# Performance work log

Measured on AMD Instinct MI355X. Metric: run time of the kernel, lower is better.

Reference implementation:

```python
import jax, jax.numpy as jnp
import numpy as np

C_IN, C_OUT, K, H = 64, 128, 27, 100000

def setup_inputs() -> dict:
    key = jax.random.key(0)
    k1, k2, k3 = jax.random.split(key, 3)
    data_in = jax.random.normal(k1, (1, C_IN, H, 1), dtype=jnp.float32)
    # neighbor index table: 27 neighbors per node; -1 would mean 'missing' (zero-padded)
    neigh = jax.random.randint(k2, (H, K), 0, H, dtype=jnp.int64)
    # conv weight, fan-in scaled init, stored [C_out, C_in, K]
    weight = jax.random.normal(k3, (C_OUT, C_IN, K), dtype=jnp.float32) / np.sqrt(C_IN * K)
    return {"data_in": data_in, "neigh": neigh, "weight": weight}

def reference(data_in, neigh, weight):
    # data_in: [1, C_in, H, 1] (ocnn layout) -> [C_in, H]
    x = data_in[0, :, :, 0]
    # octree2col: gather 27 neighbors per node -> [C_in, H, K]
    cols = x[:, neigh]
    # zero out missing neighbors (index < 0)
    cols = jnp.where(neigh[None, :, :] >= 0, cols, jnp.zeros((), dtype=cols.dtype))
    # GEMM over (C_in, K) fused with ReLU -> [C_out, H]
    out = jnp.einsum('chk,ock->oh', cols, weight)
    out = jax.nn.relu(out)
    return out[None, :, :, None]  # back to ocnn layout [1, C_out, H, 1]
```

## Files before the change

kernel.cpp:

```cpp
#include <hip/hip_runtime.h>
#include <hip/hip_bf16.h>

#define C_IN  64
#define C_OUT 128
#define KK    27
#define HH    100000
#define TB    1563
#define WB    108
#define NBLK  391

typedef __attribute__((ext_vector_type(8))) short s8v;
typedef __attribute__((ext_vector_type(4))) float f32x4;

__device__ inline unsigned short f2bf(float f) {
    __hip_bfloat16 h = __float2bfloat16(f);
    return *reinterpret_cast<unsigned short*>(&h);
}

__device__ inline void dma16(const void* g, void* l) {
    __builtin_amdgcn_global_load_lds((const __attribute__((address_space(1))) void*)g,
                                     (__attribute__((address_space(3))) void*)l, 16, 0, 0);
}

__global__ __launch_bounds__(256) void prep_kernel(const float* __restrict__ x,
                                                   const float* __restrict__ w,
                                                   unsigned short* __restrict__ xt,
                                                   unsigned short* __restrict__ wk) {
    const int tid = threadIdx.x;
    if (blockIdx.x < TB) {
        __shared__ __align__(16) unsigned short ts[64 * 72];
        const int hbase = blockIdx.x * 64;
        #pragma unroll
        for (int it = 0; it < 16; ++it) {
            int i = it * 256 + tid;
            int c = i >> 6, hl = i & 63;
            int hg = hbase + hl;
            float v = (hg < HH) ? x[(size_t)c * HH + hg] : 0.f;
            ts[hl * 72 + c] = f2bf(v);
        }
        __syncthreads();
        #pragma unroll
        for (int it = 0; it < 2; ++it) {
            int u = it * 256 + tid;
            int hl = u >> 3, part = u & 7;
            int hg = hbase + hl;
            if (hg < HH)
                *(int4*)&xt[(size_t)hg * 64 + part * 8] = *(const int4*)&ts[hl * 72 + part * 8];
        }
    } else {
        int b = blockIdx.x - TB;
        int base = b * 2048 + tid;
        #pragma unroll
        for (int j = 0; j < 8; ++j) {
            int t = base + j * 256;
            int jj = t & 63, o = (t >> 6) & 127, kx = t >> 13;
            int lc = (jj >> 3) ^ (o & 7);
            int c  = lc * 8 + (jj & 7);
            wk[t] = f2bf(w[(size_t)o * (C_IN * KK) + c * KK + kx]);
        }
    }
}

__global__ __launch_bounds__(256, 2) void conv_main(const unsigned short* __restrict__ xt,
                                                    const unsigned short* __restrict__ wk,
                                                    const int* __restrict__ neigh,
                                                    float* __restrict__ out) {
    __shared__ int neigh_s[256 * KK];
    __shared__ __align__(16) unsigned short w_s[2][128 * 64];

    const int tid  = threadIdx.x;
    const int wave = tid >> 6;
    const int lane = tid & 63;
    const int col  = lane & 15;
    const int quad = lane >> 4;
    const int hbase = blockIdx.x * 256;

    #pragma unroll
    for (int j = 0; j < KK; ++j) {
        int i = j * 256 + tid;
        int hl = i / KK, kx = i - hl * KK;
        int hg = hbase + hl;
        neigh_s[i] = (hg < HH) ? neigh[(size_t)hg * KK + kx] : -1;
    }

    {
        const unsigned short* src = wk;
        #pragma unroll
        for (int i = 0; i < 4; ++i) {
            int row_base = wave * 8 + i * 32;
            dma16(src + row_base * 64 + lane * 8, &w_s[0][row_base * 64]);
        }
    }

    f32x4 acc[8][4];
    #pragma unroll
    for (int mt = 0; mt < 8; ++mt)
        #pragma unroll
        for (int nt = 0; nt < 4; ++nt)
            acc[mt][nt] = (f32x4){0.f, 0.f, 0.f, 0.f};

    __syncthreads();

    int4 cur[2][4], nxt[2][4];
    const int pc_b = (quad * 8);
    auto loadB = [&](int kk, int4 (&frag)[2][4]) {
        #pragma unroll
        for (int nt = 0; nt < 4; ++nt) {
            int n = wave * 64 + nt * 16 + col;
            int idx = neigh_s[n * KK + kk];
            if (idx >= 0) {
                const unsigned short* base = xt + (size_t)idx * 64 + pc_b;
                frag[0][nt] = *(const int4*)(base);
                frag[1][nt] = *(const int4*)(base + 32);
            } else {
                frag[0][nt] = make_int4(0, 0, 0, 0);
                frag[1][nt] = make_int4(0, 0, 0, 0);
            }
        }
    };

    loadB(0, cur);

    int p = 0;
    #pragma unroll 1
    for (int k = 0; k < KK; ++k) {
        if (k + 1 < KK) {
            const unsigned short* src = wk + (size_t)(k + 1) * (C_OUT * C_IN);
            #pragma unroll
            for (int i = 0; i < 4; ++i) {
                int row_base = wave * 8 + i * 32;
                dma16(src + row_base * 64 + lane * 8, &w_s[p ^ 1][row_base * 64]);
            }
            loadB(k + 1, nxt);
        }

        #pragma unroll
        for (int ch = 0; ch < 2; ++ch) {
            const int pc = (ch * 4 + quad) ^ (col & 7);
            #pragma unroll
            for (int mt = 0; mt < 8; ++mt) {
                s8v a = *(const s8v*)&w_s[p][(mt * 16 + col) * 64 + pc * 8];
                #pragma unroll
                for (int nt = 0; nt < 4; ++nt) {
                    s8v b = __builtin_bit_cast(s8v, cur[ch][nt]);
                    acc[mt][nt] = __builtin_amdgcn_mfma_f32_16x16x32_bf16(a, b, acc[mt][nt], 0, 0, 0);
                }
            }
        }

        __syncthreads();
        #pragma unroll
        for (int ch = 0; ch < 2; ++ch)
            #pragma unroll
            for (int nt = 0; nt < 4; ++nt)
                cur[ch][nt] = nxt[ch][nt];
        p ^= 1;
    }

    #pragma unroll
    for (int mt = 0; mt < 8; ++mt) {
        #pragma unroll
        for (int nt = 0; nt < 4; ++nt) {
            int hg = hbase + wave * 64 + nt * 16 + col;
            if (hg < HH) {
                #pragma unroll
                for (int r = 0; r < 4; ++r) {
                    int o = mt * 16 + quad * 4 + r;
                    float v = acc[mt][nt][r];
                    out[(size_t)o * HH + hg] = v > 0.f ? v : 0.f;
                }
            }
        }
    }
}

extern "C" void kernel_launch(void* const* d_in, const int* in_sizes, int n_in,
                              void* d_out, int out_size, void* d_ws, size_t ws_size,
                              hipStream_t stream) {
    const float* data_in = (const float*)d_in[0];
    const int*   neigh   = (const int*)d_in[1];
    const float* weight  = (const float*)d_in[2];
    float* out = (float*)d_out;

    unsigned short* xt = (unsigned short*)d_ws;
    unsigned short* wk = xt + (size_t)HH * 64;

    prep_kernel<<<TB + WB, 256, 0, stream>>>(data_in, weight, xt, wk);
    conv_main<<<NBLK, 256, 0, stream>>>(xt, wk, neigh, out);
}
```

Measured before the change: 167.6 us.

## Halve per-block node tile to 128 and unroll k-loop by two for occupancy

Each block now covers 128 nodes instead of 256, which doubles the grid and halves the accumulator and B-fragment registers per wave. Launch bounds go from 2 to 3 blocks per CU. The k loop is manually unrolled by two with explicit ping-pong register buffers, so the per-iteration copy of next fragments into current ones is removed. The aim is more waves in flight to hide gather latency, at the cost of loading the weight tiles twice as many times in total and doing half the MFMA reuse of each A fragment.

```diff
diff --git a/kernel.cpp b/kernel.cpp
--- a/kernel.cpp
+++ b/kernel.cpp
@@ -7,7 +7,7 @@
 #define HH    100000
 #define TB    1563
 #define WB    108
-#define NBLK  391
+#define NBLK  782
 
 typedef __attribute__((ext_vector_type(8))) short s8v;
 typedef __attribute__((ext_vector_type(4))) float f32x4;
@@ -61,11 +61,11 @@
     }
 }
 
-__global__ __launch_bounds__(256, 2) void conv_main(const unsigned short* __restrict__ xt,
+__global__ __launch_bounds__(256, 3) void conv_main(const unsigned short* __restrict__ xt,
                                                     const unsigned short* __restrict__ wk,
                                                     const int* __restrict__ neigh,
                                                     float* __restrict__ out) {
-    __shared__ int neigh_s[256 * KK];
+    __shared__ int neigh_s[128 * KK];
     __shared__ __align__(16) unsigned short w_s[2][128 * 64];
 
     const int tid  = threadIdx.x;
@@ -73,95 +73,89 @@
     const int lane = tid & 63;
     const int col  = lane & 15;
     const int quad = lane >> 4;
-    const int hbase = blockIdx.x * 256;
+    const int hbase = blockIdx.x * 128;
 
-    #pragma unroll
-    for (int j = 0; j < KK; ++j) {
-        int i = j * 256 + tid;
+    for (int i = tid; i < 128 * KK; i += 256) {
         int hl = i / KK, kx = i - hl * KK;
         int hg = hbase + hl;
         neigh_s[i] = (hg < HH) ? neigh[(size_t)hg * KK + kx] : -1;
     }
 
-    {
-        const unsigned short* src = wk;
+    auto dmaW = [&](int k, int b) {
+        const unsigned short* src = wk + (size_t)k * (C_OUT * C_IN);
         #pragma unroll
         for (int i = 0; i < 4; ++i) {
             int row_base = wave * 8 + i * 32;
-            dma16(src + row_base * 64 + lane * 8, &w_s[0][row_base * 64]);
+            dma16(src + row_base * 64 + lane * 8, &w_s[b][row_base * 64]);
         }
+    };
+
+    dmaW(0, 0);
+
+    f32x4 acc[8][2];
+    #pragma unroll
+    for (int mt = 0; mt < 8; ++mt) {
+        acc[mt][0] = (f32x4){0.f, 0.f, 0.f, 0.f};
+        acc[mt][1] = (f32x4){0.f, 0.f, 0.f, 0.f};
     }
-
-    f32x4 acc[8][4];
-    #pragma unroll
-    for (int mt = 0; mt < 8; ++mt)
-        #pragma unroll
-        for (int nt = 0; nt < 4; ++nt)
-            acc[mt][nt] = (f32x4){0.f, 0.f, 0.f, 0.f};
 
     __syncthreads();
 
-    int4 cur[2][4], nxt[2][4];
-    const int pc_b = (quad * 8);
-    auto loadB = [&](int kk, int4 (&frag)[2][4]) {
+    const int pc_b = quad * 8;
+    auto loadB = [&](int kk, int4 (&B)[4]) {
         #pragma unroll
-        for (int nt = 0; nt < 4; ++nt) {
-            int n = wave * 64 + nt * 16 + col;
+        for (int nt = 0; nt < 2; ++nt) {
+            int n = wave * 32 + nt * 16 + col;
             int idx = neigh_s[n * KK + kk];
             if (idx >= 0) {
                 const unsigned short* base = xt + (size_t)idx * 64 + pc_b;
-                frag[0][nt] = *(const int4*)(base);
-                frag[1][nt] = *(const int4*)(base + 32);
+                B[nt]     = *(const int4*)(base);
+                B[2 + nt] = *(const int4*)(base + 32);
             } else {
-                frag[0][nt] = make_int4(0, 0, 0, 0);
-                frag[1][nt] = make_int4(0, 0, 0, 0);
+                B[nt]     = make_int4(0, 0, 0, 0);
+                B[2 + nt] = make_int4(0, 0, 0, 0);
             }
         }
     };
 
-    loadB(0, cur);
-
-    int p = 0;
-    #pragma unroll 1
-    for (int k = 0; k < KK; ++k) {
-        if (k + 1 < KK) {
-            const unsigned short* src = wk + (size_t)(k + 1) * (C_OUT * C_IN);
-            #pragma unroll
-            for (int i = 0; i < 4; ++i) {
-                int row_base = wave * 8 + i * 32;
-                dma16(src + row_base * 64 + lane * 8, &w_s[p ^ 1][row_base * 64]);
-            }
-            loadB(k + 1, nxt);
-        }
-
+    auto mfma_phase = [&](const unsigned short* wbuf, int4 (&B)[4]) {
         #pragma unroll
         for (int ch = 0; ch < 2; ++ch) {
             const int pc = (ch * 4 + quad) ^ (col & 7);
             #pragma unroll
             for (int mt = 0; mt < 8; ++mt) {
-                s8v a = *(const s8v*)&w_s[p][(mt * 16 + col) * 64 + pc * 8];
-                #pragma unroll
-                for (int nt = 0; nt < 4; ++nt) {
-                    s8v b = __builtin_bit_cast(s8v, cur[ch][nt]);
-                    acc[mt][nt] = __builtin_amdgcn_mfma_f32_16x16x32_bf16(a, b, acc[mt][nt], 0, 0, 0);
-                }
+                s8v a = *(const s8v*)&wbuf[(mt * 16 + col) * 64 + pc * 8];
+                acc[mt][0] = __builtin_amdgcn_mfma_f32_16x16x32_bf16(a, __builtin_bit_cast(s8v, B[ch * 2 + 0]), acc[mt][0], 0, 0, 0);
+                acc[mt][1] = __builtin_amdgcn_mfma_f32_16x16x32_bf16(a, __builtin_bit_cast(s8v, B[ch * 2 + 1]), acc[mt][1], 0, 0, 0);
             }
         }
+    };
 
+    int4 B0[4], B1[4];
+    loadB(0, B0);
+
+    #pragma unroll 1
+    for (int kb = 0; kb < 13; ++kb) {
+        int k = kb * 2;
+        dmaW(k + 1, 1);
+        loadB(k + 1, B1);
+        mfma_phase(w_s[0], B0);
         __syncthreads();
-        #pragma unroll
-        for (int ch = 0; ch < 2; ++ch)
-            #pragma unroll
-            for (int nt = 0; nt < 4; ++nt)
-                cur[ch][nt] = nxt[ch][nt];
-        p ^= 1;
+
+        if (k + 2 < KK) {
+            dmaW(k + 2, 0);
+            loadB(k + 2, B0);
+        }
+        mfma_phase(w_s[1], B1);
+        __syncthreads();
     }
+    mfma_phase(w_s[0], B0);
 
     #pragma unroll
     for (int mt = 0; mt < 8; ++mt) {
         #pragma unroll
-        for (int nt = 0; nt < 4; ++nt) {
-            int hg = hbase + wave * 64 + nt * 16 + col;
+        for (int nt = 0; nt < 2; ++nt) {
+            int hg = hbase + wave * 32 + nt * 16 + col;
             if (hg < HH) {
                 #pragma unroll
                 for (int r = 0; r < 4; ++r) {
```

Result: slower. 186.8 us (+11.5%).

## Replace LDS DMA weight loads with register-staged double buffer and manual barriers

Applied to the files above, without the earlier changes.

Weights are no longer loaded with global_load_lds DMA. They are loaded into registers, written to the alternate LDS buffer after each MFMA phase, and B gathers are prefetched two stages ahead. The loop is unrolled by two with ping-pong register sets, and __syncthreads is replaced by an lgkmcnt-only waitcnt plus s_barrier, so outstanding global loads are not drained at each barrier. This costs extra registers (weight staging and a second B set) and risks spills or lower occupancy under launch_bounds(256,2), plus redundant loads at the tail where the stage index is clamped.

```diff
diff --git a/kernel.cpp b/kernel.cpp
--- a/kernel.cpp
+++ b/kernel.cpp
@@ -12,14 +12,16 @@
 typedef __attribute__((ext_vector_type(8))) short s8v;
 typedef __attribute__((ext_vector_type(4))) float f32x4;
 
+#define LGKM0_BARRIER() do { \
+    __asm__ __volatile__("" ::: "memory"); \
+    __builtin_amdgcn_s_waitcnt(0xC07F); \
+    __builtin_amdgcn_s_barrier(); \
+    __asm__ __volatile__("" ::: "memory"); \
+} while (0)
+
 __device__ inline unsigned short f2bf(float f) {
     __hip_bfloat16 h = __float2bfloat16(f);
     return *reinterpret_cast<unsigned short*>(&h);
-}
-
-__device__ inline void dma16(const void* g, void* l) {
-    __builtin_amdgcn_global_load_lds((const __attribute__((address_space(1))) void*)g,
-                                     (__attribute__((address_space(3))) void*)l, 16, 0, 0);
 }
 
 __global__ __launch_bounds__(256) void prep_kernel(const float* __restrict__ x,
@@ -83,15 +85,6 @@
         neigh_s[i] = (hg < HH) ? neigh[(size_t)hg * KK + kx] : -1;
     }
 
-    {
-        const unsigned short* src = wk;
-        #pragma unroll
-        for (int i = 0; i < 4; ++i) {
-            int row_base = wave * 8 + i * 32;
-            dma16(src + row_base * 64 + lane * 8, &w_s[0][row_base * 64]);
-        }
-    }
-
     f32x4 acc[8][4];
     #pragma unroll
     for (int mt = 0; mt < 8; ++mt)
@@ -101,61 +94,81 @@
 
     __syncthreads();
 
-    int4 cur[2][4], nxt[2][4];
-    const int pc_b = (quad * 8);
-    auto loadB = [&](int kk, int4 (&frag)[2][4]) {
+    const unsigned short* xq = xt + quad * 8;
+
+    auto loadW = [&](int k, int4 (&W)[4]) {
+        const int4* src = (const int4*)(wk + (size_t)k * (C_OUT * C_IN));
+        #pragma unroll
+        for (int j = 0; j < 4; ++j) W[j] = src[j * 256 + tid];
+    };
+    auto writeW = [&](int p, int4 (&W)[4]) {
+        #pragma unroll
+        for (int j = 0; j < 4; ++j)
+            *(int4*)&w_s[p][(j * 256 + tid) * 8] = W[j];
+    };
+
+    auto loadB = [&](int kk, int4 (&B)[2][4]) {
         #pragma unroll
         for (int nt = 0; nt < 4; ++nt) {
             int n = wave * 64 + nt * 16 + col;
             int idx = neigh_s[n * KK + kk];
             if (idx >= 0) {
-                const unsigned short* base = xt + (size_t)idx * 64 + pc_b;
-                frag[0][nt] = *(const int4*)(base);
-                frag[1][nt] = *(const int4*)(base + 32);
+                const unsigned short* base = xq + (size_t)idx * 64;
+                B[0][nt] = *(const int4*)(base);
+                B[1][nt] = *(const int4*)(base + 32);
             } else {
-                frag[0][nt] = make_int4(0, 0, 0, 0);
-                frag[1][nt] = make_int4(0, 0, 0, 0);
+                B[0][nt] = make_int4(0, 0, 0, 0);
+                B[1][nt] = make_int4(0, 0, 0, 0);
             }
         }
     };
 
-    loadB(0, cur);
-
-    int p = 0;
-    #pragma unroll 1
-    for (int k = 0; k < KK; ++k) {
-        if (k + 1 < KK) {
-            const unsigned short* src = wk + (size_t)(k + 1) * (C_OUT * C_IN);
-            #pragma unroll
-            for (int i = 0; i < 4; ++i) {
-                int row_base = wave * 8 + i * 32;
-                dma16(src + row_base * 64 + lane * 8, &w_s[p ^ 1][row_base * 64]);
-            }
-            loadB(k + 1, nxt);
-        }
-
+    auto mfma_phase = [&](const unsigned short* wbuf, int4 (&B)[2][4]) {
         #pragma unroll
         for (int ch = 0; ch < 2; ++ch) {
             const int pc = (ch * 4 + quad) ^ (col & 7);
             #pragma unroll
             for (int mt = 0; mt < 8; ++mt) {
-                s8v a = *(const s8v*)&w_s[p][(mt * 16 + col) * 64 + pc * 8];
+                s8v a = *(const s8v*)&wbuf[(mt * 16 + col) * 64 + pc * 8];
                 #pragma unroll
-                for (int nt = 0; nt < 4; ++nt) {
-                    s8v b = __builtin_bit_cast(s8v, cur[ch][nt]);
-                    acc[mt][nt] = __builtin_amdgcn_mfma_f32_16x16x32_bf16(a, b, acc[mt][nt], 0, 0, 0);
-                }
+                for (int nt = 0; nt < 4; ++nt)
+                    acc[mt][nt] = __builtin_amdgcn_mfma_f32_16x16x32_bf16(
+                        a, __builtin_bit_cast(s8v, B[ch][nt]), acc[mt][nt], 0, 0, 0);
             }
         }
-
-        __syncthreads();
-        #pragma unroll
-        for (int ch = 0; ch < 2; ++ch)
-            #pragma unroll
-            for (int nt = 0; nt < 4; ++nt)
-                cur[ch][nt] = nxt[ch][nt];
-        p ^= 1;
-    }
+    };
+
+    int4 WA[4], WB_[4], B0[2][4], B1[2][4];
+
+    loadW(0, WA);
+    loadB(0, B0);
+    writeW(0, WA);
+    loadW(1, WB_);
+    loadB(1, B1);
+    LGKM0_BARRIER();
+
+    #pragma unroll 1
+    for (int kb = 0; kb < 13; ++kb) {
+        int k = kb * 2;
+        mfma_phase(w_s[0], B0);
+        writeW(1, WB_);
+        {
+            int kc = (k + 2 < KK) ? k + 2 : KK - 1;
+            loadW(kc, WA);
+            loadB(kc, B0);
+        }
+        LGKM0_BARRIER();
+
+        mfma_phase(w_s[1], B1);
+        writeW(0, WA);
+        {
+            int kc = (k + 3 < KK) ? k + 3 : KK - 1;
+            loadW(kc, WB_);
+            loadB(kc, B1);
+        }
+        LGKM0_BARRIER();
+    }
+    mfma_phase(w_s[0], B0);
 
     #pragma unroll
     for (int mt = 0; mt < 8; ++mt) {
```

Result: slower. 232.7 us (+38.9%).
